# Kernel tuning notes

Hardware: AMD Instinct MI355X
Metric: run time of the kernel (lower is better)

The kernel has to match this reference:

```python
import jax, jax.numpy as jnp
import numpy as np

MAX_ITERS = 30
NDIM = 3
TAU = 1.0 / (2.0 * NDIM)  # skimage Chambolle step size


def _grad(u, ax):
    # forward difference along ax, zero at the last slice (skimage convention)
    g = jnp.diff(u, axis=ax)
    pad = [(0, 0)] * u.ndim
    pad[ax] = (0, 1)
    return jnp.pad(g, pad)


def _div(p):
    # adjoint of _grad: d[ax] = shift_forward(p[ax]) - p[ax]
    d = jnp.zeros_like(p[0])
    for ax in range(NDIM):
        pa = p[ax]
        sl = [slice(None)] * NDIM
        sl[ax] = slice(0, -1)
        pad = [(0, 0)] * NDIM
        pad[ax] = (1, 0)
        d = d + jnp.pad(pa[tuple(sl)], pad) - pa
    return d


def tv_chambolle_nd(image, weight):
    # Chambolle projection algorithm (skimage _denoise_tv_chambolle_nd), fixed iters.
    def step(p, _):
        out = image + _div(p)
        g = jnp.stack([_grad(out, ax) for ax in range(NDIM)], axis=0)  # (3,B,T,F)
        norm = jnp.sqrt(jnp.sum(g * g, axis=0, keepdims=True))
        norm = norm * (TAU / weight) + 1.0
        return (p - TAU * g) / norm, None

    p0 = jnp.zeros((NDIM,) + image.shape, image.dtype)
    # iteration i returns out built from p after i updates; after max_iters loop
    # iterations the returned `out` used p updated (max_iters-1) times.
    p, _ = jax.lax.scan(jax.checkpoint(step), p0, None, length=MAX_ITERS - 1)
    return image + _div(p)


def setup_inputs() -> dict:
    key = jax.random.key(0)
    kx, kl, kb = jax.random.split(key, 3)
    x = jax.random.normal(kx, (8, 2048, 128), dtype=jnp.float32)
    # lambdas has a non-neg constraint; keep it strictly positive
    lambdas = jax.random.uniform(kl, (1, 1), dtype=jnp.float32) * 0.1 + 0.05
    b = jax.random.normal(kb, (1, 1, 128), dtype=jnp.float32) * 0.01
    return {"x": x, "lambdas": lambdas, "b": b}


def reference(x, lambdas, b):
    out = tv_chambolle_nd(x.astype(jnp.float32), lambdas)
    out = out + b  # use_bias=True; activation=None
    return out
```

## Files before the change

### kernel.cpp

```cpp
#include <hip/hip_runtime.h>
#include <hip/hip_fp16.h>


#define BB 8
#define TT 2048
#define FF 128
#define NV (BB*TT*FF)
#define SB (TT*FF)
#define ST FF
#define RR 8
#define NBLK (TT/RR)
#define HH 4
#define EE 16
#define GR 8

constexpr float TAU = 1.0f / 6.0f;

__device__ __forceinline__ float4 ld4(const float* p) { return *reinterpret_cast<const float4*>(p); }
__device__ __forceinline__ void st4(float* p, const float4& v) { *reinterpret_cast<float4*>(p) = v; }
__device__ __forceinline__ float4 ld4h(const __half* p) {
    uint2 u = *reinterpret_cast<const uint2*>(p);
    __half2 h0 = *reinterpret_cast<__half2*>(&u.x);
    __half2 h1 = *reinterpret_cast<__half2*>(&u.y);
    float2 a = __half22float2(h0), b2 = __half22float2(h1);
    return make_float4(a.x, a.y, b2.x, b2.y);
}
__device__ __forceinline__ void st4h(__half* p, const float4& v) {
    __half2 h0 = __float22half2_rn(make_float2(v.x, v.y));
    __half2 h1 = __float22half2_rn(make_float2(v.z, v.w));
    uint2 u;
    u.x = *reinterpret_cast<unsigned*>(&h0);
    u.y = *reinterpret_cast<unsigned*>(&h1);
    *reinterpret_cast<uint2*>(p) = u;
}
__device__ __forceinline__ float4 shfl_up4(float4 v, int d) {
    return make_float4(__shfl_up(v.x, d), __shfl_up(v.y, d), __shfl_up(v.z, d), __shfl_up(v.w, d));
}
__device__ __forceinline__ float4 shfl_dn4(float4 v, int d) {
    return make_float4(__shfl_down(v.x, d), __shfl_down(v.y, d), __shfl_down(v.z, d), __shfl_down(v.w, d));
}
__device__ __forceinline__ float4 sub4(const float4& a, const float4& b) {
    return make_float4(a.x - b.x, a.y - b.y, a.z - b.z, a.w - b.w);
}
__device__ __forceinline__ float4 f4z() { return make_float4(0.f, 0.f, 0.f, 0.f); }
__device__ __forceinline__ float4 nbvec(const float4& gB, const float4& gT, const float4& gF, float s) {
    float4 nb; float q;
    q = gB.x * gB.x + gT.x * gT.x + gF.x * gF.x;
    nb.x = __builtin_amdgcn_rcpf(fmaf(__builtin_amdgcn_sqrtf(q), s, 1.f));
    q = gB.y * gB.y + gT.y * gT.y + gF.y * gF.y;
    nb.y = __builtin_amdgcn_rcpf(fmaf(__builtin_amdgcn_sqrtf(q), s, 1.f));
    q = gB.z * gB.z + gT.z * gT.z + gF.z * gF.z;
    nb.z = __builtin_amdgcn_rcpf(fmaf(__builtin_amdgcn_sqrtf(q), s, 1.f));
    q = gB.w * gB.w + gT.w * gT.w + gF.w * gF.w;
    nb.w = __builtin_amdgcn_rcpf(fmaf(__builtin_amdgcn_sqrtf(q), s, 1.f));
    return nb;
}

struct ConeShared {
    float p2b[EE][4][8];
    float outx[EE][4][8];
    float4 p1if[256];
    float4 oif[256];
};

template<int RG>
__device__ __forceinline__ void publish(int k, float4 (&P1)[GR], float4 (&P2)[GR],
                                        ConeShared& sh, int c, int b, int fg, int w) {
    if (fg == 7) {
        #pragma unroll
        for (int le = 0; le < GR; ++le) {
            const int e = RG * GR + le;
            if (e >= k && e < EE - k) sh.p2b[e][w][b] = P2[le].w;
        }
    }
    if (RG == 0) sh.p1if[c] = P1[GR - 1];
}

template<int RG, bool ELO, bool EHI>
__device__ __forceinline__ void phase_out(
    int k, const float4 (&Xr)[GR],
    float4 (&P0)[GR], float4 (&P1)[GR], float4 (&P2)[GR], float4 (&O)[GR],
    ConeShared& sh, int c, int b, int fg, int w, int f0, int tb) {
    #pragma unroll
    for (int le = 0; le < GR; ++le) {
        const int e = RG * GR + le;
        if (e < k + 1 || e >= EE - k) continue;
        const int t = tb + e;
        if ((ELO && t < 0) || (EHI && t >= TT)) continue;
        const float4 X = Xr[le];
        float4 o;
        o.x = X.x - P0[le].x - P1[le].x - P2[le].x;
        o.y = X.y - P0[le].y - P1[le].y - P2[le].y + P2[le].x;
        o.z = X.z - P0[le].z - P1[le].z - P2[le].z + P2[le].y;
        o.w = X.w - P0[le].w - P1[le].w - P2[le].w + P2[le].z;
        float4 h0 = shfl_up4(P0[le], 1);
        if (b > 0) { o.x += h0.x; o.y += h0.y; o.z += h0.z; o.w += h0.w; }
        float4 pm1 = (le > 0) ? P1[le - 1] : sh.p1if[c];
        if (!ELO || t > 0) { o.x += pm1.x; o.y += pm1.y; o.z += pm1.z; o.w += pm1.w; }
        float pw = __shfl_up(P2[le].w, 8);
        if (fg == 0) pw = (w > 0) ? sh.p2b[e][(w - 1)][b] : 0.0f;
        if (f0 > 0) o.x += pw;
        O[le] = o;
        if (fg == 0) sh.outx[e][w][b] = o.x;
    }
}

template<int RG, bool ELO, bool EHI>
__device__ __forceinline__ void phase_upd(
    int k, float4 (&P0)[GR], float4 (&P1)[GR], float4 (&P2)[GR], float4 (&O)[GR],
    ConeShared& sh, int c, int b, int fg, int w, int f0, int tb, float s) {
    #pragma unroll
    for (int le = 0; le < GR; ++le) {
        const int e = RG * GR + le;
        if (e < k + 1 || e > EE - 2 - k) continue;
        const int t = tb + e;
        if ((ELO && t < 0) || (EHI && t >= TT)) continue;
        const float4 cc = O[le];
        const float4 on = (le < GR - 1) ? O[le + 1] : sh.oif[c];
        float4 gT = f4z();
        if (!EHI || t < TT - 1) gT = sub4(on, cc);
        const float4 nB = shfl_dn4(cc, 1);
        float4 gB = f4z();
        if (b < BB - 1) gB = sub4(nB, cc);
        float nxx = __shfl_down(cc.x, 8);
        if (fg == 7) nxx = (w < 3) ? sh.outx[e][w + 1][b] : 0.0f;
        float4 gF;
        gF.x = cc.y - cc.x;
        gF.y = cc.z - cc.y;
        gF.z = cc.w - cc.z;
        gF.w = (f0 < FF - 4) ? (nxx - cc.w) : 0.f;
        const float4 nb = nbvec(gB, gT, gF, s);
        P0[le].x = fmaf(-TAU, gB.x, P0[le].x) * nb.x;
        P0[le].y = fmaf(-TAU, gB.y, P0[le].y) * nb.y;
        P0[le].z = fmaf(-TAU, gB.z, P0[le].z) * nb.z;
        P0[le].w = fmaf(-TAU, gB.w, P0[le].w) * nb.w;
        P1[le].x = fmaf(-TAU, gT.x, P1[le].x) * nb.x;
        P1[le].y = fmaf(-TAU, gT.y, P1[le].y) * nb.y;
        P1[le].z = fmaf(-TAU, gT.z, P1[le].z) * nb.z;
        P1[le].w = fmaf(-TAU, gT.w, P1[le].w) * nb.w;
        P2[le].x = fmaf(-TAU, gF.x, P2[le].x) * nb.x;
        P2[le].y = fmaf(-TAU, gF.y, P2[le].y) * nb.y;
        P2[le].z = fmaf(-TAU, gF.z, P2[le].z) * nb.z;
        P2[le].w = fmaf(-TAU, gF.w, P2[le].w) * nb.w;
    }
}

template<bool ELO, bool EHI>
__device__ __forceinline__ void cone_run(
    const float4 (&Xr)[GR],
    float4 (&P0)[GR], float4 (&P1)[GR], float4 (&P2)[GR], float4 (&O)[GR],
    ConeShared& sh, int rg, int c, int b, int fg, int w, int f0, int tb, float s) {
    #pragma unroll
    for (int k = 0; k < HH; ++k) {
        if (rg == 0) publish<0>(k, P1, P2, sh, c, b, fg, w);
        else         publish<1>(k, P1, P2, sh, c, b, fg, w);
        __syncthreads();
        if (rg == 0) phase_out<0, ELO, EHI>(k, Xr, P0, P1, P2, O, sh, c, b, fg, w, f0, tb);
        else         phase_out<1, ELO, EHI>(k, Xr, P0, P1, P2, O, sh, c, b, fg, w, f0, tb);
        if (rg == 1) sh.oif[c] = O[0];
        __syncthreads();
        if (rg == 0) phase_upd<0, ELO, EHI>(k, P0, P1, P2, O, sh, c, b, fg, w, f0, tb, s);
        else         phase_upd<1, ELO, EHI>(k, P0, P1, P2, O, sh, c, b, fg, w, f0, tb, s);
    }
}

template<bool ELO, bool EHI>
__device__ __forceinline__ void mid_main(
    const float* __restrict__ x, const __half* __restrict__ pin, __half* __restrict__ pout,
    ConeShared& sh, int rg, int c, int b, int fg, int w, int f0, int tb, int e0,
    int base, float s) {
    float4 P0[GR], P1[GR], P2[GR], O[GR], Xr[GR];
    #pragma unroll
    for (int le = 0; le < GR; ++le) {
        const int t = tb + e0 + le;
        const bool ok = (!ELO || t >= 0) && (!EHI || t < TT);
        const bool trim = (rg == 0 && le == 0);
        if (ok) {
            const int v = base + t * ST;
            P1[le] = ld4h(pin + NV + v);
            if (!trim) {
                P0[le] = ld4h(pin + v);
                P2[le] = ld4h(pin + 2 * NV + v);
                Xr[le] = ld4(x + v);
            } else { P0[le] = f4z(); P2[le] = f4z(); Xr[le] = f4z(); }
        } else {
            P0[le] = f4z(); P1[le] = f4z(); P2[le] = f4z(); Xr[le] = f4z();
        }
        O[le] = f4z();
    }
    cone_run<ELO, EHI>(Xr, P0, P1, P2, O, sh, rg, c, b, fg, w, f0, tb, s);
    #pragma unroll
    for (int le = 0; le < GR; ++le) {
        const int e = e0 + le;
        if (e >= HH && e < HH + RR) {
            const int v = base + (tb + e) * ST;
            st4h(pout + v, P0[le]);
            st4h(pout + NV + v, P1[le]);
            st4h(pout + 2 * NV + v, P2[le]);
        }
    }
}

__global__ __launch_bounds__(512, 2)
void k_mid(const float* __restrict__ x, const __half* __restrict__ pin,
           __half* __restrict__ pout, const float* __restrict__ lam) {
    __shared__ ConeShared sh;
    const int tid = threadIdx.x;
    const int blk = blockIdx.x;
    const int rg  = tid >> 8;
    const int c   = tid & 255;
    const int b   = tid & 7;
    const int fg  = (tid >> 3) & 7;
    const int w   = (tid >> 6) & 3;
    const int f0  = w * 32 + fg * 4;
    const int tb  = blk * RR - HH;
    const int e0  = rg * GR;
    const int base = b * SB + f0;
    const float s = TAU / lam[0];
    if (blk == 0 || blk == NBLK - 1)
        mid_main<true, true>(x, pin, pout, sh, rg, c, b, fg, w, f0, tb, e0, base, s);
    else
        mid_main<false, false>(x, pin, pout, sh, rg, c, b, fg, w, f0, tb, e0, base, s);
}

template<bool ELO, bool EHI>
__device__ __forceinline__ void first_main(
    const float* __restrict__ x, __half* __restrict__ pout,
    ConeShared& sh, int rg, int c, int b, int fg, int w, int f0, int tb, int e0,
    int base, float s) {
    float4 P0[GR], P1[GR], P2[GR], O[GR], Xr[GR], XHa;
    #pragma unroll
    for (int le = 0; le < GR; ++le) {
        const int t = tb + e0 + le;
        const bool ok = (!ELO || t >= 0) && (!EHI || t < TT);
        Xr[le] = ok ? ld4(x + base + t * ST) : f4z();
        O[le] = f4z();
    }
    {
        const int t = tb + e0 + GR;
        const bool ok = (!ELO || t >= 0) && (t < TT);
        XHa = ok ? ld4(x + base + t * ST) : f4z();
    }
    #pragma unroll
    for (int le = 0; le < GR; ++le) {
        const int t = tb + e0 + le;
        if ((!ELO || t >= 0) && (!EHI || t < TT)) {
            const float4 cc = Xr[le];
            const float4 nxt = (le < GR - 1) ? Xr[le + 1] : XHa;
            float4 gT = f4z();
            if (t < TT - 1) gT = sub4(nxt, cc);
            const float4 nB = shfl_dn4(cc, 1);
            float4 gB = f4z();
            if (b < BB - 1) gB = sub4(nB, cc);
            float4 gF;
            gF.x = cc.y - cc.x;
            gF.y = cc.z - cc.y;
            gF.z = cc.w - cc.z;
            gF.w = (f0 < FF - 4) ? (x[base + t * ST + 4] - cc.w) : 0.f;
            const float4 nb = nbvec(gB, gT, gF, s);
            P0[le] = make_float4(-TAU * gB.x * nb.x, -TAU * gB.y * nb.y,
                                 -TAU * gB.z * nb.z, -TAU * gB.w * nb.w);
            P1[le] = make_float4(-TAU * gT.x * nb.x, -TAU * gT.y * nb.y,
                                 -TAU * gT.z * nb.z, -TAU * gT.w * nb.w);
            P2[le] = make_float4(-TAU * gF.x * nb.x, -TAU * gF.y * nb.y,
                                 -TAU * gF.z * nb.z, -TAU * gF.w * nb.w);
        } else {
            P0[le] = f4z(); P1[le] = f4z(); P2[le] = f4z();
        }
    }
    cone_run<ELO, EHI>(Xr, P0, P1, P2, O, sh, rg, c, b, fg, w, f0, tb, s);
    #pragma unroll
    for (int le = 0; le < GR; ++le) {
        const int e = e0 + le;
        if (e >= HH && e < HH + RR) {
            const int v = base + (tb + e) * ST;
            st4h(pout + v, P0[le]);
            st4h(pout + NV + v, P1[le]);
            st4h(pout + 2 * NV + v, P2[le]);
        }
    }
}

__global__ __launch_bounds__(512, 2)
void k_first(const float* __restrict__ x, __half* __restrict__ pout,
             const float* __restrict__ lam) {
    __shared__ ConeShared sh;
    const int tid = threadIdx.x;
    const int blk = blockIdx.x;
    const int rg  = tid >> 8;
    const int c   = tid & 255;
    const int b   = tid & 7;
    const int fg  = (tid >> 3) & 7;
    const int w   = (tid >> 6) & 3;
    const int f0  = w * 32 + fg * 4;
    const int tb  = blk * RR - HH;
    const int e0  = rg * GR;
    const int base = b * SB + f0;
    const float s = TAU / lam[0];
    if (blk == 0 || blk == NBLK - 1)
        first_main<true, true>(x, pout, sh, rg, c, b, fg, w, f0, tb, e0, base, s);
    else
        first_main<false, false>(x, pout, sh, rg, c, b, fg, w, f0, tb, e0, base, s);
}

__global__ __launch_bounds__(256)
void k_final(const float* __restrict__ x, const __half* __restrict__ pin,
             const float* __restrict__ bias, float* __restrict__ out) {
    const int gid = blockIdx.x * 256 + threadIdx.x;
    const int v = gid * 4;
    const int f0 = v & (FF - 1);
    const int t = (v >> 7) & (TT - 1);
    const int b = v >> 18;
    const __half* p0 = pin;
    const __half* p1 = pin + NV;
    const __half* p2 = pin + 2 * NV;
    float4 X = ld4(x + v);
    float4 a0 = ld4h(p0 + v), a1 = ld4h(p1 + v), a2 = ld4h(p2 + v);
    float ox = X.x - a0.x - a1.x - a2.x;
    float oy = X.y - a0.y - a1.y - a2.y + a2.x;
    float oz = X.z - a0.z - a1.z - a2.z + a2.y;
    float ow = X.w - a0.w - a1.w - a2.w + a2.z;
    if (b > 0) { float4 h = ld4h(p0 + v - SB); ox += h.x; oy += h.y; oz += h.z; ow += h.w; }
    if (t > 0) { float4 h = ld4h(p1 + v - ST); ox += h.x; oy += h.y; oz += h.z; ow += h.w; }
    if (f0 > 0) ox += __half2float(p2[v - 1]);
    float4 bi = ld4(bias + f0);
    st4(out + v, make_float4(ox + bi.x, oy + bi.y, oz + bi.z, ow + bi.w));
}

extern "C" void kernel_launch(void* const* d_in, const int* in_sizes, int n_in,
                              void* d_out, int out_size, void* d_ws, size_t ws_size,
                              hipStream_t stream) {
    const float* x    = (const float*)d_in[0];
    const float* lam  = (const float*)d_in[1];
    const float* bias = (const float*)d_in[2];
    float* out = (float*)d_out;

    __half* pA = (__half*)d_ws;
    __half* pB = pA + 3 * NV;

    k_first<<<NBLK, 512, 0, stream>>>(x, pA, lam);
    __half* pin = pA;
    __half* pout = pB;
    for (int i = 0; i < 6; ++i) {
        k_mid<<<NBLK, 512, 0, stream>>>(x, pin, pout, lam);
        __half* tmp = pin; pin = pout; pout = tmp;
    }
    k_final<<<NV / 1024, 256, 0, stream>>>(x, pin, bias, out);
}
```

Baseline: 255.9 us.

## Widen temporal-blocking cone to five iterations per launch with three row groups

The halo is enlarged from 4 to 5 rows, giving a cone of 18 time rows split across three 256-thread groups of 6 rows each, so the block size grows to 768 threads. Each mid launch now fuses 5 Chambolle iterations instead of 4. The schedule becomes first(5) + 4×mid(5) + mid(3), six launches instead of seven, which cuts global fp16 p round-trips. In exchange each launch does more redundant halo computation and has a third group, and the higher thread count and launch bound change register pressure and occupancy.

Result: slower. 375.5 us (+46.7%).

```diff
diff --git a/kernel.cpp b/kernel.cpp
--- a/kernel.cpp
+++ b/kernel.cpp
@@ -10,9 +10,11 @@
 #define ST FF
 #define RR 8
 #define NBLK (TT/RR)
-#define HH 4
-#define EE 16
-#define GR 8
+#define EE 18
+#define GR 6
+#define NG 3
+#define NTHR 768
+#define MARGIN 5
 
 constexpr float TAU = 1.0f / 6.0f;
 
@@ -59,8 +61,8 @@
 struct ConeShared {
     float p2b[EE][4][8];
     float outx[EE][4][8];
-    float4 p1if[256];
-    float4 oif[256];
+    float4 p1if[NG - 1][256];
+    float4 oif[NG - 1][256];
 };
 
 template<int RG>
@@ -73,7 +75,7 @@
             if (e >= k && e < EE - k) sh.p2b[e][w][b] = P2[le].w;
         }
     }
-    if (RG == 0) sh.p1if[c] = P1[GR - 1];
+    if (RG < NG - 1) sh.p1if[RG][c] = P1[GR - 1];
 }
 
 template<int RG, bool ELO, bool EHI>
@@ -95,7 +97,7 @@
         o.w = X.w - P0[le].w - P1[le].w - P2[le].w + P2[le].z;
         float4 h0 = shfl_up4(P0[le], 1);
         if (b > 0) { o.x += h0.x; o.y += h0.y; o.z += h0.z; o.w += h0.w; }
-        float4 pm1 = (le > 0) ? P1[le - 1] : sh.p1if[c];
+        float4 pm1 = (le > 0) ? P1[le - 1] : sh.p1if[RG == 0 ? 0 : RG - 1][c];
         if (!ELO || t > 0) { o.x += pm1.x; o.y += pm1.y; o.z += pm1.z; o.w += pm1.w; }
         float pw = __shfl_up(P2[le].w, 8);
         if (fg == 0) pw = (w > 0) ? sh.p2b[e][(w - 1)][b] : 0.0f;
@@ -116,7 +118,7 @@
         const int t = tb + e;
         if ((ELO && t < 0) || (EHI && t >= TT)) continue;
         const float4 cc = O[le];
-        const float4 on = (le < GR - 1) ? O[le + 1] : sh.oif[c];
+        const float4 on = (le < GR - 1) ? O[le + 1] : sh.oif[RG < NG - 1 ? RG : 0][c];
         float4 gT = f4z();
         if (!EHI || t < TT - 1) gT = sub4(on, cc);
         const float4 nB = shfl_dn4(cc, 1);
@@ -145,26 +147,44 @@
     }
 }
 
-template<bool ELO, bool EHI>
+template<int HHt, bool ELO, bool EHI>
 __device__ __forceinline__ void cone_run(
     const float4 (&Xr)[GR],
     float4 (&P0)[GR], float4 (&P1)[GR], float4 (&P2)[GR], float4 (&O)[GR],
     ConeShared& sh, int rg, int c, int b, int fg, int w, int f0, int tb, float s) {
     #pragma unroll
-    for (int k = 0; k < HH; ++k) {
-        if (rg == 0) publish<0>(k, P1, P2, sh, c, b, fg, w);
-        else         publish<1>(k, P1, P2, sh, c, b, fg, w);
+    for (int k = 0; k < HHt; ++k) {
+        if (rg == 0)      publish<0>(k, P1, P2, sh, c, b, fg, w);
+        else if (rg == 1) publish<1>(k, P1, P2, sh, c, b, fg, w);
+        else              publish<2>(k, P1, P2, sh, c, b, fg, w);
         __syncthreads();
-        if (rg == 0) phase_out<0, ELO, EHI>(k, Xr, P0, P1, P2, O, sh, c, b, fg, w, f0, tb);
-        else         phase_out<1, ELO, EHI>(k, Xr, P0, P1, P2, O, sh, c, b, fg, w, f0, tb);
-        if (rg == 1) sh.oif[c] = O[0];
+        if (rg == 0)      phase_out<0, ELO, EHI>(k, Xr, P0, P1, P2, O, sh, c, b, fg, w, f0, tb);
+        else if (rg == 1) phase_out<1, ELO, EHI>(k, Xr, P0, P1, P2, O, sh, c, b, fg, w, f0, tb);
+        else              phase_out<2, ELO, EHI>(k, Xr, P0, P1, P2, O, sh, c, b, fg, w, f0, tb);
+        if (rg > 0) sh.oif[rg - 1][c] = O[0];
         __syncthreads();
-        if (rg == 0) phase_upd<0, ELO, EHI>(k, P0, P1, P2, O, sh, c, b, fg, w, f0, tb, s);
-        else         phase_upd<1, ELO, EHI>(k, P0, P1, P2, O, sh, c, b, fg, w, f0, tb, s);
-    }
-}
-
-template<bool ELO, bool EHI>
+        if (rg == 0)      phase_upd<0, ELO, EHI>(k, P0, P1, P2, O, sh, c, b, fg, w, f0, tb, s);
+        else if (rg == 1) phase_upd<1, ELO, EHI>(k, P0, P1, P2, O, sh, c, b, fg, w, f0, tb, s);
+        else              phase_upd<2, ELO, EHI>(k, P0, P1, P2, O, sh, c, b, fg, w, f0, tb, s);
+    }
+}
+
+__device__ __forceinline__ void store_owned(
+    __half* __restrict__ pout, const float4 (&P0)[GR], const float4 (&P1)[GR],
+    const float4 (&P2)[GR], int e0, int tb, int base) {
+    #pragma unroll
+    for (int le = 0; le < GR; ++le) {
+        const int e = e0 + le;
+        if (e >= MARGIN && e < MARGIN + RR) {
+            const int v = base + (tb + e) * ST;
+            st4h(pout + v, P0[le]);
+            st4h(pout + NV + v, P1[le]);
+            st4h(pout + 2 * NV + v, P2[le]);
+        }
+    }
+}
+
+template<int HHt, bool ELO, bool EHI>
 __device__ __forceinline__ void mid_main(
     const float* __restrict__ x, const __half* __restrict__ pin, __half* __restrict__ pout,
     ConeShared& sh, int rg, int c, int b, int fg, int w, int f0, int tb, int e0,
@@ -188,20 +208,12 @@
         }
         O[le] = f4z();
     }
-    cone_run<ELO, EHI>(Xr, P0, P1, P2, O, sh, rg, c, b, fg, w, f0, tb, s);
-    #pragma unroll
-    for (int le = 0; le < GR; ++le) {
-        const int e = e0 + le;
-        if (e >= HH && e < HH + RR) {
-            const int v = base + (tb + e) * ST;
-            st4h(pout + v, P0[le]);
-            st4h(pout + NV + v, P1[le]);
-            st4h(pout + 2 * NV + v, P2[le]);
-        }
-    }
-}
-
-__global__ __launch_bounds__(512, 2)
+    cone_run<HHt, ELO, EHI>(Xr, P0, P1, P2, O, sh, rg, c, b, fg, w, f0, tb, s);
+    store_owned(pout, P0, P1, P2, e0, tb, base);
+}
+
+template<int HHt>
+__global__ __launch_bounds__(NTHR, 3)
 void k_mid(const float* __restrict__ x, const __half* __restrict__ pin,
            __half* __restrict__ pout, const float* __restrict__ lam) {
     __shared__ ConeShared sh;
@@ -213,14 +225,14 @@
     const int fg  = (tid >> 3) & 7;
     const int w   = (tid >> 6) & 3;
     const int f0  = w * 32 + fg * 4;
-    const int tb  = blk * RR - HH;
+    const int tb  = blk * RR - MARGIN;
     const int e0  = rg * GR;
     const int base = b * SB + f0;
     const float s = TAU / lam[0];
     if (blk == 0 || blk == NBLK - 1)
-        mid_main<true, true>(x, pin, pout, sh, rg, c, b, fg, w, f0, tb, e0, base, s);
+        mid_main<HHt, true, true>(x, pin, pout, sh, rg, c, b, fg, w, f0, tb, e0, base, s);
     else
-        mid_main<false, false>(x, pin, pout, sh, rg, c, b, fg, w, f0, tb, e0, base, s);
+        mid_main<HHt, false, false>(x, pin, pout, sh, rg, c, b, fg, w, f0, tb, e0, base, s);
 }
 
 template<bool ELO, bool EHI>
@@ -268,20 +280,11 @@
             P0[le] = f4z(); P1[le] = f4z(); P2[le] = f4z();
         }
     }
-    cone_run<ELO, EHI>(Xr, P0, P1, P2, O, sh, rg, c, b, fg, w, f0, tb, s);
-    #pragma unroll
-    for (int le = 0; le < GR; ++le) {
-        const int e = e0 + le;
-        if (e >= HH && e < HH + RR) {
-            const int v = base + (tb + e) * ST;
-            st4h(pout + v, P0[le]);
-            st4h(pout + NV + v, P1[le]);
-            st4h(pout + 2 * NV + v, P2[le]);
-        }
-    }
-}
-
-__global__ __launch_bounds__(512, 2)
+    cone_run<MARGIN, ELO, EHI>(Xr, P0, P1, P2, O, sh, rg, c, b, fg, w, f0, tb, s);
+    store_owned(pout, P0, P1, P2, e0, tb, base);
+}
+
+__global__ __launch_bounds__(NTHR, 3)
 void k_first(const float* __restrict__ x, __half* __restrict__ pout,
              const float* __restrict__ lam) {
     __shared__ ConeShared sh;
@@ -293,7 +296,7 @@
     const int fg  = (tid >> 3) & 7;
     const int w   = (tid >> 6) & 3;
     const int f0  = w * 32 + fg * 4;
-    const int tb  = blk * RR - HH;
+    const int tb  = blk * RR - MARGIN;
     const int e0  = rg * GR;
     const int base = b * SB + f0;
     const float s = TAU / lam[0];
@@ -338,12 +341,16 @@
     __half* pA = (__half*)d_ws;
     __half* pB = pA + 3 * NV;
 
-    k_first<<<NBLK, 512, 0, stream>>>(x, pA, lam);
+    k_first<<<NBLK, NTHR, 0, stream>>>(x, pA, lam);
     __half* pin = pA;
     __half* pout = pB;
-    for (int i = 0; i < 6; ++i) {
-        k_mid<<<NBLK, 512, 0, stream>>>(x, pin, pout, lam);
+    for (int i = 0; i < 4; ++i) {
+        k_mid<5><<<NBLK, NTHR, 0, stream>>>(x, pin, pout, lam);
         __half* tmp = pin; pin = pout; pout = tmp;
     }
+    k_mid<3><<<NBLK, NTHR, 0, stream>>>(x, pin, pout, lam);
+    {
+        __half* tmp = pin; pin = pout; pout = tmp;
+    }
     k_final<<<NV / 1024, 256, 0, stream>>>(x, pin, bias, out);
 }
```
